# Performance work log

Hardware: AMD Instinct MI355X
Metric: run time of the kernel (lower is better)

Reference implementation:

```python
import jax, jax.numpy as jnp
import numpy as np

N_NODES = 40000
N_EDGES = 640000
N_FEAT = 128
HIDDEN = 128
N_GRAPHS = 64


def _sage_conv(x, src, dst, Wl, b, Wr):
    # PyG SAGEConv (aggr='mean', root_weight=True, normalize=False):
    # out_i = W_l @ mean_{j in N(i)} x_j + b + W_r @ x_i
    msg = x[src]                                             # [E, F]
    s = jax.ops.segment_sum(msg, dst, num_segments=N_NODES)  # [N, F]
    deg = jax.ops.segment_sum(jnp.ones((src.shape[0],), x.dtype), dst,
                              num_segments=N_NODES)
    agg = s / jnp.maximum(deg, 1.0)[:, None]
    return agg @ Wl + b + x @ Wr


def setup_inputs() -> dict:
    key = jax.random.key(0)
    ks = jax.random.split(key, 12)
    sc = 1.0 / np.sqrt(N_FEAT)
    x = jax.random.normal(ks[0], (N_NODES, N_FEAT), dtype=jnp.float32)
    edge_index = jax.random.randint(ks[1], (2, N_EDGES), 0, N_NODES, dtype=jnp.int32)
    batch = jnp.sort(jax.random.randint(ks[2], (N_NODES,), 0, N_GRAPHS, dtype=jnp.int32))
    mk = lambda k, shp: (jax.random.normal(k, shp, dtype=jnp.float32) * sc)
    return {
        'x': x, 'edge_index': edge_index, 'batch': batch,
        'W1l': mk(ks[3], (N_FEAT, HIDDEN)), 'b1': jnp.zeros((HIDDEN,), jnp.float32),
        'W1r': mk(ks[4], (N_FEAT, HIDDEN)),
        'W2l': mk(ks[5], (HIDDEN, HIDDEN)), 'b2': jnp.zeros((HIDDEN,), jnp.float32),
        'W2r': mk(ks[6], (HIDDEN, HIDDEN)),
        'W3l': mk(ks[7], (HIDDEN, HIDDEN)), 'b3': jnp.zeros((HIDDEN,), jnp.float32),
        'W3r': mk(ks[8], (HIDDEN, HIDDEN)),
        'Wlin': mk(ks[9], (3 * HIDDEN, HIDDEN)), 'blin': jnp.zeros((HIDDEN,), jnp.float32),
    }


def reference(x, edge_index, batch, W1l, b1, W1r, W2l, b2, W2r, W3l, b3, W3r, Wlin, blin):
    src, dst = edge_index[0], edge_index[1]
    h1 = jax.nn.relu(_sage_conv(x, src, dst, W1l, b1, W1r))
    h2 = jax.nn.relu(_sage_conv(h1, src, dst, W2l, b2, W2r))
    h3 = jax.nn.relu(_sage_conv(h2, src, dst, W3l, b3, W3r))
    h = jnp.concatenate([h1, h2, h3], axis=1)                # [N, 3*H]
    pooled = jax.ops.segment_sum(h, batch, num_segments=N_GRAPHS)  # global_add_pool
    out = jax.nn.relu(pooled @ Wlin + blin)                  # [G, H]
    return out
```

## Files before the change

kernel.cpp:

```cpp
#include <hip/hip_runtime.h>
#include <hip/hip_bf16.h>

#define N_NODES 40000
#define N_EDGES 640000
#define NFEAT 128
#define NGRAPHS 64

typedef __attribute__((ext_vector_type(8))) short short8;
typedef __attribute__((ext_vector_type(4))) float float4v;

static __device__ __forceinline__ float bf2f(unsigned short u) {
    unsigned int x = ((unsigned int)u) << 16;
    return __builtin_bit_cast(float, x);
}
static __device__ __forceinline__ unsigned short f2bf(float f) {
    unsigned int x = __builtin_bit_cast(unsigned int, f);
    unsigned int r = x + 0x7fffu + ((x >> 16) & 1u);
    return (unsigned short)(r >> 16);
}

__global__ void k_count(const int* __restrict__ dst, int* __restrict__ deg) {
    int e = blockIdx.x * 256 + threadIdx.x;
    if (e < N_EDGES) atomicAdd(&deg[dst[e]], 1);
}

__global__ __launch_bounds__(1024) void k_scan1(const int* __restrict__ deg,
                                                int* __restrict__ offsets,
                                                int* __restrict__ bsum) {
    __shared__ int ws[16];
    int tid = threadIdx.x;
    int i = blockIdx.x * 1024 + tid;
    int v = (i < N_NODES) ? deg[i] : 0;
    int lane = tid & 63, wave = tid >> 6;
    int incl = v;
    for (int d = 1; d < 64; d <<= 1) {
        int t = __shfl_up(incl, d, 64);
        if (lane >= d) incl += t;
    }
    if (lane == 63) ws[wave] = incl;
    __syncthreads();
    if (wave == 0 && lane < 16) {
        int w = ws[lane];
        for (int d = 1; d < 16; d <<= 1) {
            int t = __shfl_up(w, d, 64);
            if (lane >= d) w += t;
        }
        ws[lane] = w;
    }
    __syncthreads();
    int waveOff = (wave == 0) ? 0 : ws[wave - 1];
    if (i < N_NODES) offsets[i] = waveOff + incl - v;
    if (tid == 1023) bsum[blockIdx.x] = ws[15];
}

__global__ __launch_bounds__(1024) void k_scan3(const int* __restrict__ bsum,
                                                int* __restrict__ offsets,
                                                int* __restrict__ cursor) {
    __shared__ int s_boff;
    int tid = threadIdx.x;
    if (tid < 64) {
        int v = (tid < 40) ? bsum[tid] : 0;
        int incl = v;
        for (int d = 1; d < 64; d <<= 1) {
            int t = __shfl_up(incl, d, 64);
            if (tid >= d) incl += t;
        }
        int excl = incl - v;
        int my = __shfl(excl, blockIdx.x, 64);
        if (tid == 0) s_boff = my;
    }
    __syncthreads();
    int boff = s_boff;
    int i = blockIdx.x * 1024 + tid;
    if (i < N_NODES) {
        int o = offsets[i] + boff;
        offsets[i] = o;
        cursor[i]  = o;
    }
    if (blockIdx.x == 0 && tid == 0) offsets[N_NODES] = N_EDGES;
}

__global__ void k_fill(const int* __restrict__ src, const int* __restrict__ dst,
                       int* __restrict__ cursor, int* __restrict__ esrc) {
    int e = blockIdx.x * 256 + threadIdx.x;
    if (e < N_EDGES) {
        int d = dst[e];
        int p = atomicAdd(&cursor[d], 1);
        esrc[p] = src[e];
    }
}

__global__ void k_goff(const int* __restrict__ batch, int* __restrict__ goff) {
    int i = blockIdx.x * 256 + threadIdx.x;
    if (i >= N_NODES) return;
    int b1 = batch[i];
    int b0 = (i == 0) ? -1 : batch[i - 1];
    for (int g = b0 + 1; g <= b1; ++g) goff[g] = i;
    if (i == N_NODES - 1)
        for (int g = b1 + 1; g <= NGRAPHS; ++g) goff[g] = N_NODES;
}

__global__ void k_castx(const float* __restrict__ x, unsigned short* __restrict__ h0) {
    int i = blockIdx.x * 256 + threadIdx.x;
    const int n = N_NODES * NFEAT / 2;
    if (i < n) {
        float a = x[2 * i], b = x[2 * i + 1];
        unsigned int u = (unsigned int)f2bf(a) | ((unsigned int)f2bf(b) << 16);
        ((unsigned int*)h0)[i] = u;
    }
}

__global__ void k_castw(const float* __restrict__ Wl0, const float* __restrict__ Wr0,
                        const float* __restrict__ Wl1, const float* __restrict__ Wr1,
                        const float* __restrict__ Wl2, const float* __restrict__ Wr2,
                        unsigned short* __restrict__ Wt) {
    int id = blockIdx.x * 256 + threadIdx.x;
    if (id >= 3 * 128 * 256) return;
    int l   = id >> 15;
    int rem = id & 32767;
    int nn  = rem >> 8;
    int k   = rem & 255;
    const float* Wl = (l == 0) ? Wl0 : (l == 1) ? Wl1 : Wl2;
    const float* Wr = (l == 0) ? Wr0 : (l == 1) ? Wr1 : Wr2;
    float v = (k < 128) ? Wl[k * 128 + nn] : Wr[(k - 128) * 128 + nn];
    Wt[id] = f2bf(v);
}

__global__ void k_agg(const unsigned short* __restrict__ hin,
                      const int* __restrict__ offsets,
                      const int* __restrict__ esrc,
                      unsigned short* __restrict__ agg) {
    int wave = threadIdx.x >> 6;
    int lane = threadIdx.x & 63;
    int node = blockIdx.x * 4 + wave;
    if (node >= N_NODES) return;
    int beg = offsets[node], end = offsets[node + 1];
    int deg = end - beg;
    int grp = lane >> 4;
    int sub = lane & 15;
    int nb = deg < 64 ? deg : 64;
    int sj = (lane < nb) ? esrc[beg + lane] : 0;

    float a[8];
    for (int i = 0; i < 8; ++i) a[i] = 0.f;
    auto acc8 = [&](uint4 u) {
        a[0] += bf2f((unsigned short)(u.x & 0xffffu));
        a[1] += bf2f((unsigned short)(u.x >> 16));
        a[2] += bf2f((unsigned short)(u.y & 0xffffu));
        a[3] += bf2f((unsigned short)(u.y >> 16));
        a[4] += bf2f((unsigned short)(u.z & 0xffffu));
        a[5] += bf2f((unsigned short)(u.z >> 16));
        a[6] += bf2f((unsigned short)(u.w & 0xffffu));
        a[7] += bf2f((unsigned short)(u.w >> 16));
    };

    int base = 0;
    for (; base + 8 <= nb; base += 8) {
        int s0 = __shfl(sj, base + grp, 64);
        int s1 = __shfl(sj, base + grp + 4, 64);
        uint4 u0 = *(const uint4*)(hin + (size_t)s0 * 128 + sub * 8);
        uint4 u1 = *(const uint4*)(hin + (size_t)s1 * 128 + sub * 8);
        acc8(u0);
        acc8(u1);
    }
    {
        int j0 = base + grp;
        int j1 = base + grp + 4;
        int s0 = __shfl(sj, j0 & 63, 64);
        int s1 = __shfl(sj, j1 & 63, 64);
        if (j0 < nb) {
            uint4 u = *(const uint4*)(hin + (size_t)s0 * 128 + sub * 8);
            acc8(u);
        }
        if (j1 < nb) {
            uint4 u = *(const uint4*)(hin + (size_t)s1 * 128 + sub * 8);
            acc8(u);
        }
    }
    for (int t = beg + 64 + grp; t < end; t += 4) {
        int s = esrc[t];
        uint4 u = *(const uint4*)(hin + (size_t)s * 128 + sub * 8);
        acc8(u);
    }

    for (int i = 0; i < 8; ++i) {
        a[i] += __shfl_xor(a[i], 16, 64);
        a[i] += __shfl_xor(a[i], 32, 64);
    }
    float inv = 1.f / (float)(deg > 1 ? deg : 1);
    if (grp == 0) {
        uint4 v;
        v.x = (unsigned int)f2bf(a[0] * inv) | ((unsigned int)f2bf(a[1] * inv) << 16);
        v.y = (unsigned int)f2bf(a[2] * inv) | ((unsigned int)f2bf(a[3] * inv) << 16);
        v.z = (unsigned int)f2bf(a[4] * inv) | ((unsigned int)f2bf(a[5] * inv) << 16);
        v.w = (unsigned int)f2bf(a[6] * inv) | ((unsigned int)f2bf(a[7] * inv) << 16);
        *(uint4*)(agg + (size_t)node * 128 + sub * 8) = v;
    }
}

__global__ void k_gemm(const unsigned short* __restrict__ agg,
                       const unsigned short* __restrict__ hin,
                       const unsigned short* __restrict__ Wt,
                       const float* __restrict__ bias,
                       unsigned short* __restrict__ hout) {
    __shared__ __align__(16) unsigned short As[64][264];
    int tid = threadIdx.x;
    int row0 = blockIdx.x * 64;

    {
        int c  = tid & 31;
        int r0 = tid >> 5;
        for (int p = 0; p < 8; ++p) {
            int r = r0 + p * 8;
            int grow = row0 + r;
            const unsigned short* srcp = (c < 16) ? (agg + (size_t)grow * 128 + c * 8)
                                                  : (hin + (size_t)grow * 128 + (c - 16) * 8);
            uint4 v = *(const uint4*)srcp;
            *(uint4*)(&As[r][c * 8]) = v;
        }
    }
    __syncthreads();

    int wave = tid >> 6, lane = tid & 63;
    int quad = lane >> 4, l16 = lane & 15;
    float4v acc[4][2];
    for (int rt = 0; rt < 4; ++rt)
        for (int ct = 0; ct < 2; ++ct) acc[rt][ct] = {0.f, 0.f, 0.f, 0.f};

    int ncol0 = wave * 32;
    for (int kc = 0; kc < 8; ++kc) {
        int k0 = kc * 32 + quad * 8;
        short8 a[4], b[2];
        for (int rt = 0; rt < 4; ++rt)
            a[rt] = *(const short8*)(&As[rt * 16 + l16][k0]);
        for (int ct = 0; ct < 2; ++ct)
            b[ct] = *(const short8*)(Wt + (size_t)(ncol0 + ct * 16 + l16) * 256 + k0);
        for (int rt = 0; rt < 4; ++rt)
            for (int ct = 0; ct < 2; ++ct)
                acc[rt][ct] = __builtin_amdgcn_mfma_f32_16x16x32_bf16(
                    a[rt], b[ct], acc[rt][ct], 0, 0, 0);
    }

    for (int ct = 0; ct < 2; ++ct) {
        int col = ncol0 + ct * 16 + l16;
        float bv = bias[col];
        for (int rt = 0; rt < 4; ++rt) {
            int r0 = rt * 16 + quad * 4;
            for (int i = 0; i < 4; ++i) {
                float v = acc[rt][ct][i] + bv;
                v = v > 0.f ? v : 0.f;
                hout[(size_t)(row0 + r0 + i) * 128 + col] = f2bf(v);
            }
        }
    }
}

__global__ __launch_bounds__(256) void k_pool(const unsigned short* __restrict__ h1,
                                              const unsigned short* __restrict__ h2,
                                              const unsigned short* __restrict__ h3,
                                              const int* __restrict__ goff,
                                              float* __restrict__ pooled) {
    __shared__ float red[4][16][8];
    int b = blockIdx.x;
    int g = b / 3, aidx = b % 3;
    const unsigned short* h = (aidx == 0) ? h1 : (aidx == 1) ? h2 : h3;
    int beg = goff[g], end = goff[g + 1];
    int tid = threadIdx.x;
    int rp = tid >> 4;
    int ch = tid & 15;
    float a[8];
    for (int i = 0; i < 8; ++i) a[i] = 0.f;
    for (int r = beg + rp; r < end; r += 16) {
        uint4 u = *(const uint4*)(h + (size_t)r * 128 + ch * 8);
        a[0] += bf2f((unsigned short)(u.x & 0xffffu));
        a[1] += bf2f((unsigned short)(u.x >> 16));
        a[2] += bf2f((unsigned short)(u.y & 0xffffu));
        a[3] += bf2f((unsigned short)(u.y >> 16));
        a[4] += bf2f((unsigned short)(u.z & 0xffffu));
        a[5] += bf2f((unsigned short)(u.z >> 16));
        a[6] += bf2f((unsigned short)(u.w & 0xffffu));
        a[7] += bf2f((unsigned short)(u.w >> 16));
    }
    for (int i = 0; i < 8; ++i) {
        a[i] += __shfl_xor(a[i], 16, 64);
        a[i] += __shfl_xor(a[i], 32, 64);
    }
    int wave = tid >> 6, lane = tid & 63;
    if (lane < 16)
        for (int i = 0; i < 8; ++i) red[wave][lane][i] = a[i];
    __syncthreads();
    if (tid < 128) {
        int ch2 = tid >> 3, e = tid & 7;
        float s = red[0][ch2][e] + red[1][ch2][e] + red[2][ch2][e] + red[3][ch2][e];
        pooled[g * 384 + aidx * 128 + ch2 * 8 + e] = s;
    }
}

__global__ void k_final(const float* __restrict__ pooled,
                        const float* __restrict__ Wlin,
                        const float* __restrict__ blin,
                        float* __restrict__ out) {
    int g = blockIdx.x, col = threadIdx.x;
    float acc = blin[col];
    for (int k = 0; k < 384; ++k)
        acc = fmaf(pooled[g * 384 + k], Wlin[k * 128 + col], acc);
    out[g * 128 + col] = acc > 0.f ? acc : 0.f;
}

extern "C" void kernel_launch(void* const* d_in, const int* in_sizes, int n_in,
                              void* d_out, int out_size, void* d_ws, size_t ws_size,
                              hipStream_t stream) {
    const float* x    = (const float*)d_in[0];
    const int*   ei   = (const int*)d_in[1];
    const int*   src  = ei;
    const int*   dst  = ei + N_EDGES;
    const int*   batch = (const int*)d_in[2];
    const float* W1l = (const float*)d_in[3];
    const float* b1  = (const float*)d_in[4];
    const float* W1r = (const float*)d_in[5];
    const float* W2l = (const float*)d_in[6];
    const float* b2  = (const float*)d_in[7];
    const float* W2r = (const float*)d_in[8];
    const float* W3l = (const float*)d_in[9];
    const float* b3  = (const float*)d_in[10];
    const float* W3r = (const float*)d_in[11];
    const float* Wlin = (const float*)d_in[12];
    const float* blin = (const float*)d_in[13];
    float* out = (float*)d_out;

    char* ws = (char*)d_ws;
    size_t off = 0;
    auto alloc = [&](size_t bytes) -> char* {
        char* p = ws + off;
        off = (off + bytes + 255) & ~(size_t)255;
        return p;
    };
    int* offsets = (int*)alloc((N_NODES + 1) * sizeof(int));
    int* cursor  = (int*)alloc(N_NODES * sizeof(int));
    int* deg     = (int*)alloc(N_NODES * sizeof(int));
    int* bsum    = (int*)alloc(64 * sizeof(int));
    int* goff    = (int*)alloc((NGRAPHS + 1) * sizeof(int));
    int* esrc    = (int*)alloc(N_EDGES * sizeof(int));
    unsigned short* h0   = (unsigned short*)alloc((size_t)N_NODES * 128 * 2);
    unsigned short* h1   = (unsigned short*)alloc((size_t)N_NODES * 128 * 2);
    unsigned short* h2   = (unsigned short*)alloc((size_t)N_NODES * 128 * 2);
    unsigned short* h3   = (unsigned short*)alloc((size_t)N_NODES * 128 * 2);
    unsigned short* aggb = (unsigned short*)alloc((size_t)N_NODES * 128 * 2);
    unsigned short* Wt   = (unsigned short*)alloc(3 * 256 * 128 * 2);
    float* pooled = (float*)alloc(NGRAPHS * 384 * sizeof(float));

    hipMemsetAsync(deg, 0, N_NODES * sizeof(int), stream);

    k_count<<<(N_EDGES + 255) / 256, 256, 0, stream>>>(dst, deg);
    k_scan1<<<40, 1024, 0, stream>>>(deg, offsets, bsum);
    k_scan3<<<40, 1024, 0, stream>>>(bsum, offsets, cursor);
    k_fill<<<(N_EDGES + 255) / 256, 256, 0, stream>>>(src, dst, cursor, esrc);
    k_goff<<<(N_NODES + 255) / 256, 256, 0, stream>>>(batch, goff);
    k_castx<<<(N_NODES * 64 + 255) / 256, 256, 0, stream>>>(x, h0);
    k_castw<<<384, 256, 0, stream>>>(W1l, W1r, W2l, W2r, W3l, W3r, Wt);

    k_agg<<<N_NODES / 4, 256, 0, stream>>>(h0, offsets, esrc, aggb);
    k_gemm<<<625, 256, 0, stream>>>(aggb, h0, Wt, b1, h1);
    k_agg<<<N_NODES / 4, 256, 0, stream>>>(h1, offsets, esrc, aggb);
    k_gemm<<<625, 256, 0, stream>>>(aggb, h1, Wt + 32768, b2, h2);
    k_agg<<<N_NODES / 4, 256, 0, stream>>>(h2, offsets, esrc, aggb);
    k_gemm<<<625, 256, 0, stream>>>(aggb, h2, Wt + 2 * 32768, b3, h3);

    k_pool<<<3 * NGRAPHS, 256, 0, stream>>>(h1, h2, h3, goff, pooled);
    k_final<<<NGRAPHS, 128, 0, stream>>>(pooled, Wlin, blin, out);
}
```

Measured before the change: 288.3 us.

## Fuse neighbor aggregation into GEMM kernel and merge setup kernels

Aggregation of neighbor features now happens inside the GEMM kernel: each 256-thread block gathers and averages neighbors for its 64 rows straight into shared memory, which removes the intermediate agg buffer and its global write and read. The count and goff kernels are merged into one launch, as are the x and weight cast kernels, which cuts the launch count. The cost is parallelism: the gather now runs in only 625 blocks, with 16 threads per node and serial edge loops, where it used to run in 10000 blocks with one wave per node. That may hurt latency hiding on the random gathers.

```diff
diff --git a/kernel.cpp b/kernel.cpp
--- a/kernel.cpp
+++ b/kernel.cpp
@@ -19,9 +19,21 @@
     return (unsigned short)(r >> 16);
 }
 
-__global__ void k_count(const int* __restrict__ dst, int* __restrict__ deg) {
-    int e = blockIdx.x * 256 + threadIdx.x;
-    if (e < N_EDGES) atomicAdd(&deg[dst[e]], 1);
+__global__ void k_count_goff(const int* __restrict__ dst, int* __restrict__ deg,
+                             const int* __restrict__ batch, int* __restrict__ goff) {
+    int b = blockIdx.x;
+    if (b < 2500) {
+        int e = b * 256 + threadIdx.x;
+        if (e < N_EDGES) atomicAdd(&deg[dst[e]], 1);
+    } else {
+        int i = (b - 2500) * 256 + threadIdx.x;
+        if (i >= N_NODES) return;
+        int b1 = batch[i];
+        int b0 = (i == 0) ? -1 : batch[i - 1];
+        for (int g = b0 + 1; g <= b1; ++g) goff[g] = i;
+        if (i == N_NODES - 1)
+            for (int g = b1 + 1; g <= NGRAPHS; ++g) goff[g] = N_NODES;
+    }
 }
 
 __global__ __launch_bounds__(1024) void k_scan1(const int* __restrict__ deg,
@@ -90,133 +102,93 @@
     }
 }
 
-__global__ void k_goff(const int* __restrict__ batch, int* __restrict__ goff) {
-    int i = blockIdx.x * 256 + threadIdx.x;
-    if (i >= N_NODES) return;
-    int b1 = batch[i];
-    int b0 = (i == 0) ? -1 : batch[i - 1];
-    for (int g = b0 + 1; g <= b1; ++g) goff[g] = i;
-    if (i == N_NODES - 1)
-        for (int g = b1 + 1; g <= NGRAPHS; ++g) goff[g] = N_NODES;
-}
-
-__global__ void k_castx(const float* __restrict__ x, unsigned short* __restrict__ h0) {
-    int i = blockIdx.x * 256 + threadIdx.x;
-    const int n = N_NODES * NFEAT / 2;
-    if (i < n) {
-        float a = x[2 * i], b = x[2 * i + 1];
-        unsigned int u = (unsigned int)f2bf(a) | ((unsigned int)f2bf(b) << 16);
-        ((unsigned int*)h0)[i] = u;
-    }
-}
-
-__global__ void k_castw(const float* __restrict__ Wl0, const float* __restrict__ Wr0,
-                        const float* __restrict__ Wl1, const float* __restrict__ Wr1,
-                        const float* __restrict__ Wl2, const float* __restrict__ Wr2,
-                        unsigned short* __restrict__ Wt) {
-    int id = blockIdx.x * 256 + threadIdx.x;
-    if (id >= 3 * 128 * 256) return;
-    int l   = id >> 15;
-    int rem = id & 32767;
-    int nn  = rem >> 8;
-    int k   = rem & 255;
-    const float* Wl = (l == 0) ? Wl0 : (l == 1) ? Wl1 : Wl2;
-    const float* Wr = (l == 0) ? Wr0 : (l == 1) ? Wr1 : Wr2;
-    float v = (k < 128) ? Wl[k * 128 + nn] : Wr[(k - 128) * 128 + nn];
-    Wt[id] = f2bf(v);
-}
-
-__global__ void k_agg(const unsigned short* __restrict__ hin,
-                      const int* __restrict__ offsets,
-                      const int* __restrict__ esrc,
-                      unsigned short* __restrict__ agg) {
-    int wave = threadIdx.x >> 6;
-    int lane = threadIdx.x & 63;
-    int node = blockIdx.x * 4 + wave;
-    if (node >= N_NODES) return;
-    int beg = offsets[node], end = offsets[node + 1];
-    int deg = end - beg;
-    int grp = lane >> 4;
-    int sub = lane & 15;
-    int nb = deg < 64 ? deg : 64;
-    int sj = (lane < nb) ? esrc[beg + lane] : 0;
-
-    float a[8];
-    for (int i = 0; i < 8; ++i) a[i] = 0.f;
-    auto acc8 = [&](uint4 u) {
-        a[0] += bf2f((unsigned short)(u.x & 0xffffu));
-        a[1] += bf2f((unsigned short)(u.x >> 16));
-        a[2] += bf2f((unsigned short)(u.y & 0xffffu));
-        a[3] += bf2f((unsigned short)(u.y >> 16));
-        a[4] += bf2f((unsigned short)(u.z & 0xffffu));
-        a[5] += bf2f((unsigned short)(u.z >> 16));
-        a[6] += bf2f((unsigned short)(u.w & 0xffffu));
-        a[7] += bf2f((unsigned short)(u.w >> 16));
-    };
-
-    int base = 0;
-    for (; base + 8 <= nb; base += 8) {
-        int s0 = __shfl(sj, base + grp, 64);
-        int s1 = __shfl(sj, base + grp + 4, 64);
-        uint4 u0 = *(const uint4*)(hin + (size_t)s0 * 128 + sub * 8);
-        uint4 u1 = *(const uint4*)(hin + (size_t)s1 * 128 + sub * 8);
-        acc8(u0);
-        acc8(u1);
-    }
-    {
-        int j0 = base + grp;
-        int j1 = base + grp + 4;
-        int s0 = __shfl(sj, j0 & 63, 64);
-        int s1 = __shfl(sj, j1 & 63, 64);
-        if (j0 < nb) {
-            uint4 u = *(const uint4*)(hin + (size_t)s0 * 128 + sub * 8);
-            acc8(u);
-        }
-        if (j1 < nb) {
-            uint4 u = *(const uint4*)(hin + (size_t)s1 * 128 + sub * 8);
-            acc8(u);
-        }
-    }
-    for (int t = beg + 64 + grp; t < end; t += 4) {
-        int s = esrc[t];
-        uint4 u = *(const uint4*)(hin + (size_t)s * 128 + sub * 8);
-        acc8(u);
-    }
-
-    for (int i = 0; i < 8; ++i) {
-        a[i] += __shfl_xor(a[i], 16, 64);
-        a[i] += __shfl_xor(a[i], 32, 64);
-    }
-    float inv = 1.f / (float)(deg > 1 ? deg : 1);
-    if (grp == 0) {
-        uint4 v;
-        v.x = (unsigned int)f2bf(a[0] * inv) | ((unsigned int)f2bf(a[1] * inv) << 16);
-        v.y = (unsigned int)f2bf(a[2] * inv) | ((unsigned int)f2bf(a[3] * inv) << 16);
-        v.z = (unsigned int)f2bf(a[4] * inv) | ((unsigned int)f2bf(a[5] * inv) << 16);
-        v.w = (unsigned int)f2bf(a[6] * inv) | ((unsigned int)f2bf(a[7] * inv) << 16);
-        *(uint4*)(agg + (size_t)node * 128 + sub * 8) = v;
-    }
-}
-
-__global__ void k_gemm(const unsigned short* __restrict__ agg,
-                       const unsigned short* __restrict__ hin,
-                       const unsigned short* __restrict__ Wt,
-                       const float* __restrict__ bias,
-                       unsigned short* __restrict__ hout) {
+__global__ void k_cast(const float* __restrict__ x, unsigned short* __restrict__ h0,
+                       const float* __restrict__ Wl0, const float* __restrict__ Wr0,
+                       const float* __restrict__ Wl1, const float* __restrict__ Wr1,
+                       const float* __restrict__ Wl2, const float* __restrict__ Wr2,
+                       unsigned short* __restrict__ Wt) {
+    int b = blockIdx.x;
+    if (b < 10000) {
+        int i = b * 256 + threadIdx.x;
+        const int n = N_NODES * NFEAT / 2;
+        if (i < n) {
+            float a = x[2 * i], c = x[2 * i + 1];
+            unsigned int u = (unsigned int)f2bf(a) | ((unsigned int)f2bf(c) << 16);
+            ((unsigned int*)h0)[i] = u;
+        }
+    } else {
+        int id = (b - 10000) * 256 + threadIdx.x;
+        if (id >= 3 * 128 * 256) return;
+        int l   = id >> 15;
+        int rem = id & 32767;
+        int nn  = rem >> 8;
+        int k   = rem & 255;
+        const float* Wl = (l == 0) ? Wl0 : (l == 1) ? Wl1 : Wl2;
+        const float* Wr = (l == 0) ? Wr0 : (l == 1) ? Wr1 : Wr2;
+        float v = (k < 128) ? Wl[k * 128 + nn] : Wr[(k - 128) * 128 + nn];
+        Wt[id] = f2bf(v);
+    }
+}
+
+__global__ __launch_bounds__(256) void k_sage(
+        const unsigned short* __restrict__ hin,
+        const int* __restrict__ offsets,
+        const int* __restrict__ esrc,
+        const unsigned short* __restrict__ Wt,
+        const float* __restrict__ bias,
+        unsigned short* __restrict__ hout) {
     __shared__ __align__(16) unsigned short As[64][264];
     int tid = threadIdx.x;
     int row0 = blockIdx.x * 64;
 
+    for (int p = 0; p < 4; ++p) {
+        int ci = tid + p * 256;
+        int r = ci >> 4, c8 = ci & 15;
+        uint4 v = *(const uint4*)(hin + (size_t)(row0 + r) * 128 + c8 * 8);
+        *(uint4*)(&As[r][128 + c8 * 8]) = v;
+    }
+
     {
-        int c  = tid & 31;
-        int r0 = tid >> 5;
-        for (int p = 0; p < 8; ++p) {
-            int r = r0 + p * 8;
-            int grow = row0 + r;
-            const unsigned short* srcp = (c < 16) ? (agg + (size_t)grow * 128 + c * 8)
-                                                  : (hin + (size_t)grow * 128 + (c - 16) * 8);
-            uint4 v = *(const uint4*)srcp;
-            *(uint4*)(&As[r][c * 8]) = v;
+        int grp = tid >> 4;
+        int sub = tid & 15;
+        for (int nn = 0; nn < 4; ++nn) {
+            int r = nn * 16 + grp;
+            int node = row0 + r;
+            int beg = offsets[node], end = offsets[node + 1];
+            float a[8];
+            for (int i = 0; i < 8; ++i) a[i] = 0.f;
+            auto acc8 = [&](uint4 u) {
+                a[0] += bf2f((unsigned short)(u.x & 0xffffu));
+                a[1] += bf2f((unsigned short)(u.x >> 16));
+                a[2] += bf2f((unsigned short)(u.y & 0xffffu));
+                a[3] += bf2f((unsigned short)(u.y >> 16));
+                a[4] += bf2f((unsigned short)(u.z & 0xffffu));
+                a[5] += bf2f((unsigned short)(u.z >> 16));
+                a[6] += bf2f((unsigned short)(u.w & 0xffffu));
+                a[7] += bf2f((unsigned short)(u.w >> 16));
+            };
+            int j = beg;
+            for (; j + 4 <= end; j += 4) {
+                int s0 = esrc[j], s1 = esrc[j + 1], s2 = esrc[j + 2], s3 = esrc[j + 3];
+                uint4 u0 = *(const uint4*)(hin + (size_t)s0 * 128 + sub * 8);
+                uint4 u1 = *(const uint4*)(hin + (size_t)s1 * 128 + sub * 8);
+                uint4 u2 = *(const uint4*)(hin + (size_t)s2 * 128 + sub * 8);
+                uint4 u3 = *(const uint4*)(hin + (size_t)s3 * 128 + sub * 8);
+                acc8(u0); acc8(u1); acc8(u2); acc8(u3);
+            }
+            for (; j < end; ++j) {
+                int s = esrc[j];
+                uint4 u = *(const uint4*)(hin + (size_t)s * 128 + sub * 8);
+                acc8(u);
+            }
+            int deg = end - beg;
+            float inv = 1.f / (float)(deg > 1 ? deg : 1);
+            uint4 v;
+            v.x = (unsigned int)f2bf(a[0] * inv) | ((unsigned int)f2bf(a[1] * inv) << 16);
+            v.y = (unsigned int)f2bf(a[2] * inv) | ((unsigned int)f2bf(a[3] * inv) << 16);
+            v.z = (unsigned int)f2bf(a[4] * inv) | ((unsigned int)f2bf(a[5] * inv) << 16);
+            v.w = (unsigned int)f2bf(a[6] * inv) | ((unsigned int)f2bf(a[7] * inv) << 16);
+            *(uint4*)(&As[r][sub * 8]) = v;
         }
     }
     __syncthreads();
@@ -345,26 +317,20 @@
     unsigned short* h1   = (unsigned short*)alloc((size_t)N_NODES * 128 * 2);
     unsigned short* h2   = (unsigned short*)alloc((size_t)N_NODES * 128 * 2);
     unsigned short* h3   = (unsigned short*)alloc((size_t)N_NODES * 128 * 2);
-    unsigned short* aggb = (unsigned short*)alloc((size_t)N_NODES * 128 * 2);
     unsigned short* Wt   = (unsigned short*)alloc(3 * 256 * 128 * 2);
     float* pooled = (float*)alloc(NGRAPHS * 384 * sizeof(float));
 
     hipMemsetAsync(deg, 0, N_NODES * sizeof(int), stream);
 
-    k_count<<<(N_EDGES + 255) / 256, 256, 0, stream>>>(dst, deg);
+    k_count_goff<<<2657, 256, 0, stream>>>(dst, deg, batch, goff);
     k_scan1<<<40, 1024, 0, stream>>>(deg, offsets, bsum);
     k_scan3<<<40, 1024, 0, stream>>>(bsum, offsets, cursor);
     k_fill<<<(N_EDGES + 255) / 256, 256, 0, stream>>>(src, dst, cursor, esrc);
-    k_goff<<<(N_NODES + 255) / 256, 256, 0, stream>>>(batch, goff);
-    k_castx<<<(N_NODES * 64 + 255) / 256, 256, 0, stream>>>(x, h0);
-    k_castw<<<384, 256, 0, stream>>>(W1l, W1r, W2l, W2r, W3l, W3r, Wt);
-
-    k_agg<<<N_NODES / 4, 256, 0, stream>>>(h0, offsets, esrc, aggb);
-    k_gemm<<<625, 256, 0, stream>>>(aggb, h0, Wt, b1, h1);
-    k_agg<<<N_NODES / 4, 256, 0, stream>>>(h1, offsets, esrc, aggb);
-    k_gemm<<<625, 256, 0, stream>>>(aggb, h1, Wt + 32768, b2, h2);
-    k_agg<<<N_NODES / 4, 256, 0, stream>>>(h2, offsets, esrc, aggb);
-    k_gemm<<<625, 256, 0, stream>>>(aggb, h2, Wt + 2 * 32768, b3, h3);
+    k_cast<<<10384, 256, 0, stream>>>(x, h0, W1l, W1r, W2l, W2r, W3l, W3r, Wt);
+
+    k_sage<<<625, 256, 0, stream>>>(h0, offsets, esrc, Wt,             b1, h1);
+    k_sage<<<625, 256, 0, stream>>>(h1, offsets, esrc, Wt + 32768,     b2, h2);
+    k_sage<<<625, 256, 0, stream>>>(h2, offsets, esrc, Wt + 2 * 32768, b3, h3);
 
     k_pool<<<3 * NGRAPHS, 256, 0, stream>>>(h1, h2, h3, goff, pooled);
     k_final<<<NGRAPHS, 128, 0, stream>>>(pooled, Wlin, blin, out);
```

Result: no change. 291.6 us (+1.1%).
